# Kernel tuning notes

Hardware: AMD Instinct MI355X
Metric: run time of the kernel (lower is better)

The kernel has to match this reference:

```python
import jax, jax.numpy as jnp
import numpy as np

TSHAPE = (256, 256, 1024)
RANK = 32


def setup_inputs() -> dict:
    key = jax.random.key(0)
    k0, k1, k2 = jax.random.split(key, 3)
    # Nonnegative factor matrices, columns normalized to sum to 1 (as in NTF.__init__
    # via reinit_mode + norm_mode_within_factor).
    W0 = jax.random.uniform(k0, (TSHAPE[0], RANK), dtype=jnp.float32)
    W1 = jax.random.uniform(k1, (TSHAPE[1], RANK), dtype=jnp.float32)
    W2 = jax.random.uniform(k2, (TSHAPE[2], RANK), dtype=jnp.float32)
    W0 = W0 / W0.sum(axis=0)
    W1 = W1 / W1.sum(axis=0)
    W2 = W2 / W2.sum(axis=0)
    return {"W0": W0, "W1": W1, "W2": W2}


def reference(W0, W1, W2):
    # CP reconstruction: outer_prod(modes).sum(axis=-1)
    # == sum_r W0[:, r] (x) W1[:, r] (x) W2[:, r]  -> shape TSHAPE
    # einsum fuses the rank reduction, avoiding the (i, j, k, r) intermediate.
    return jnp.einsum("ir,jr,kr->ijk", W0, W1, W2)
```

## Files before the change

### kernel.cpp

```cpp
#include <hip/hip_runtime.h>


constexpr int I_DIM  = 256;
constexpr int J_DIM  = 256;
constexpr int K_DIM  = 1024;
constexpr int RNK    = 32;
constexpr int TOT_ROWS = I_DIM * J_DIM;
constexpr int GRID     = 768;

typedef float f32x2 __attribute__((ext_vector_type(2)));
typedef float f32x4 __attribute__((ext_vector_type(4)));

#if defined(__has_builtin)
#  if __has_builtin(__builtin_elementwise_fma)
#    define PK_FMA(a, b, c) __builtin_elementwise_fma((a), (b), (c))
#  endif
#endif

__device__ __forceinline__ f32x2 fma2(f32x2 a, f32x2 b, f32x2 c) {
#ifdef PK_FMA
    return PK_FMA(a, b, c);
#else
    f32x2 r;
    r.x = fmaf(a.x, b.x, c.x);
    r.y = fmaf(a.y, b.y, c.y);
    return r;
#endif
}

__global__ void transpose_w2(const float* __restrict__ W2, float* __restrict__ W2T) {
    int idx = blockIdx.x * 256 + threadIdx.x;
    int r = idx >> 10;
    int k = idx & (K_DIM - 1);
    W2T[r * K_DIM + k] = W2[k * RNK + r];
}

__global__ void precompute_c(const float* __restrict__ W0, const float* __restrict__ W1,
                             float* __restrict__ C) {
    int idx = blockIdx.x * 256 + threadIdx.x;
    int r = idx & 31;
    int j = (idx >> 5) & 255;
    int i = idx >> 13;
    C[idx] = W0[i * RNK + r] * W1[j * RNK + r];
}

__global__ __launch_bounds__(256, 3) void cp_recon_gs(const float* __restrict__ C,
                                                      const float* __restrict__ W2T,
                                                      float* __restrict__ out) {
    const int k = threadIdx.x * 4;

    f32x2 wlo[RNK], whi[RNK];
#pragma unroll
    for (int r = 0; r < RNK; ++r) {
        f32x4 t = *reinterpret_cast<const f32x4*>(&W2T[r * K_DIM + k]);
        wlo[r] = t.lo;
        whi[r] = t.hi;
    }

#pragma unroll 2
    for (int row = blockIdx.x; row < TOT_ROWS; row += GRID) {
        const float* __restrict__ cj = C + (size_t)row * RNK;
        f32x2 a0 = {0.f, 0.f}, a1 = {0.f, 0.f};
#pragma unroll
        for (int r = 0; r < RNK; ++r) {
            float s = cj[r];
            f32x2 sv = {s, s};
            a0 = fma2(sv, wlo[r], a0);
            a1 = fma2(sv, whi[r], a1);
        }
        f32x4 t;
        t.lo = a0;
        t.hi = a1;
        *reinterpret_cast<f32x4*>(out + (size_t)row * K_DIM + k) = t;
    }
}

constexpr int JT = 8;
__global__ __launch_bounds__(256, 4) void cp_recon_d(const float* __restrict__ W0,
                                                     const float* __restrict__ W1,
                                                     const float* __restrict__ W2,
                                                     float* __restrict__ out) {
    __shared__ __align__(16) float c[JT][RNK];
    const int i     = blockIdx.x >> 5;
    const int jbase = (blockIdx.x & 31) * JT;
    const int tid   = threadIdx.x;

    if (tid < JT * RNK) {
        int jj = tid >> 5;
        int r  = tid & 31;
        c[jj][r] = W0[i * RNK + r] * W1[(jbase + jj) * RNK + r];
    }
    __syncthreads();

    const int k = tid * 4;
    float4 acc[JT];
#pragma unroll
    for (int jj = 0; jj < JT; ++jj) acc[jj] = make_float4(0.f, 0.f, 0.f, 0.f);

    for (int rc = 0; rc < RNK; rc += 4) {
        float4 row[4];
#pragma unroll
        for (int q = 0; q < 4; ++q)
            row[q] = *reinterpret_cast<const float4*>(&W2[(k + q) * RNK + rc]);
#pragma unroll
        for (int jj = 0; jj < JT; ++jj) {
            float4 c4 = *reinterpret_cast<const float4*>(&c[jj][rc]);
            acc[jj].x = fmaf(c4.x, row[0].x, fmaf(c4.y, row[0].y, fmaf(c4.z, row[0].z, fmaf(c4.w, row[0].w, acc[jj].x))));
            acc[jj].y = fmaf(c4.x, row[1].x, fmaf(c4.y, row[1].y, fmaf(c4.z, row[1].z, fmaf(c4.w, row[1].w, acc[jj].y))));
            acc[jj].z = fmaf(c4.x, row[2].x, fmaf(c4.y, row[2].y, fmaf(c4.z, row[2].z, fmaf(c4.w, row[2].w, acc[jj].z))));
            acc[jj].w = fmaf(c4.x, row[3].x, fmaf(c4.y, row[3].y, fmaf(c4.z, row[3].z, fmaf(c4.w, row[3].w, acc[jj].w))));
        }
    }
#pragma unroll
    for (int jj = 0; jj < JT; ++jj) {
        int o = (i * J_DIM + jbase + jj) * K_DIM + k;
        *reinterpret_cast<float4*>(&out[o]) = acc[jj];
    }
}

extern "C" void kernel_launch(void* const* d_in, const int* in_sizes, int n_in,
                              void* d_out, int out_size, void* d_ws, size_t ws_size,
                              hipStream_t stream) {
    const float* W0 = (const float*)d_in[0];
    const float* W1 = (const float*)d_in[1];
    const float* W2 = (const float*)d_in[2];
    float* out = (float*)d_out;

    const size_t w2t_bytes = (size_t)RNK * K_DIM * sizeof(float);
    const size_t c_bytes   = (size_t)I_DIM * J_DIM * RNK * sizeof(float);

    if (ws_size >= w2t_bytes + c_bytes) {
        float* W2T  = (float*)d_ws;
        float* Cbuf = (float*)((char*)d_ws + w2t_bytes);
        transpose_w2<<<(RNK * K_DIM) / 256, 256, 0, stream>>>(W2, W2T);
        precompute_c<<<(I_DIM * J_DIM * RNK) / 256, 256, 0, stream>>>(W0, W1, Cbuf);
        cp_recon_gs<<<GRID, 256, 0, stream>>>(Cbuf, W2T, out);
    } else {
        cp_recon_d<<<I_DIM * (J_DIM / JT), 256, 0, stream>>>(W0, W1, W2, out);
    }
}
```

Measured before the change: 66.37 us.

## Fuse W0*W1 product into reconstruction kernel, folding W1 into register-held W2

Removes the precompute kernel that built the full I×J×R C buffer in workspace. Each block's j stays fixed because the grid stride is a multiple of J, so W1[j] is multiplied into the register-resident W2 columns once. The inner loop then reads W0 rows directly. This avoids a kernel launch and the write and read-back of the intermediate buffer, and the result depends on the grid being a multiple of J.

```diff
diff --git a/kernel.cpp b/kernel.cpp
--- a/kernel.cpp
+++ b/kernel.cpp
@@ -35,35 +35,31 @@
     W2T[r * K_DIM + k] = W2[k * RNK + r];
 }
 
-__global__ void precompute_c(const float* __restrict__ W0, const float* __restrict__ W1,
-                             float* __restrict__ C) {
-    int idx = blockIdx.x * 256 + threadIdx.x;
-    int r = idx & 31;
-    int j = (idx >> 5) & 255;
-    int i = idx >> 13;
-    C[idx] = W0[i * RNK + r] * W1[j * RNK + r];
-}
-
-__global__ __launch_bounds__(256, 3) void cp_recon_gs(const float* __restrict__ C,
+__global__ __launch_bounds__(256, 3) void cp_recon_fw(const float* __restrict__ W0,
+                                                      const float* __restrict__ W1,
                                                       const float* __restrict__ W2T,
                                                       float* __restrict__ out) {
     const int k = threadIdx.x * 4;
+    const int j = blockIdx.x & (J_DIM - 1);
 
     f32x2 wlo[RNK], whi[RNK];
 #pragma unroll
     for (int r = 0; r < RNK; ++r) {
         f32x4 t = *reinterpret_cast<const f32x4*>(&W2T[r * K_DIM + k]);
-        wlo[r] = t.lo;
-        whi[r] = t.hi;
+        float u = W1[j * RNK + r];
+        f32x2 uv = {u, u};
+        wlo[r] = t.lo * uv;
+        whi[r] = t.hi * uv;
     }
 
 #pragma unroll 2
     for (int row = blockIdx.x; row < TOT_ROWS; row += GRID) {
-        const float* __restrict__ cj = C + (size_t)row * RNK;
+        const int i = row >> 8;
+        const float* __restrict__ c0 = W0 + (size_t)i * RNK;
         f32x2 a0 = {0.f, 0.f}, a1 = {0.f, 0.f};
 #pragma unroll
         for (int r = 0; r < RNK; ++r) {
-            float s = cj[r];
+            float s = c0[r];
             f32x2 sv = {s, s};
             a0 = fma2(sv, wlo[r], a0);
             a1 = fma2(sv, whi[r], a1);
@@ -127,14 +123,11 @@
     float* out = (float*)d_out;
 
     const size_t w2t_bytes = (size_t)RNK * K_DIM * sizeof(float);
-    const size_t c_bytes   = (size_t)I_DIM * J_DIM * RNK * sizeof(float);
 
-    if (ws_size >= w2t_bytes + c_bytes) {
-        float* W2T  = (float*)d_ws;
-        float* Cbuf = (float*)((char*)d_ws + w2t_bytes);
+    if (ws_size >= w2t_bytes) {
+        float* W2T = (float*)d_ws;
         transpose_w2<<<(RNK * K_DIM) / 256, 256, 0, stream>>>(W2, W2T);
-        precompute_c<<<(I_DIM * J_DIM * RNK) / 256, 256, 0, stream>>>(W0, W1, Cbuf);
-        cp_recon_gs<<<GRID, 256, 0, stream>>>(Cbuf, W2T, out);
+        cp_recon_fw<<<GRID, 256, 0, stream>>>(W0, W1, W2T, out);
     } else {
         cp_recon_d<<<I_DIM * (J_DIM / JT), 256, 0, stream>>>(W0, W1, W2, out);
     }
```

New measurement: 67.91 us. 2.3% more time.
